# Kernel tuning notes

Measured on AMD Instinct MI355X. Metric: run time of the kernel, lower is better.

The kernel has to match this reference:

```python
import jax, jax.numpy as jnp
import numpy as np

LAG = 5
MSG_HID = 256
N_ATOMS = 30
N_EDGES = N_ATOMS * (N_ATOMS - 1)  # 870
BATCH = 2
T = 200


def _rel_matrices():
    # fully-connected directed graph, no self loops (standard NRI encoding)
    recv, send = [], []
    for i in range(N_ATOMS):
        for j in range(N_ATOMS):
            if i != j:
                recv.append(i)
                send.append(j)
    rel_rec = np.zeros((N_EDGES, N_ATOMS), dtype=np.float32)
    rel_send = np.zeros((N_EDGES, N_ATOMS), dtype=np.float32)
    rel_rec[np.arange(N_EDGES), recv] = 1.0
    rel_send[np.arange(N_EDGES), send] = 1.0
    return jnp.asarray(rel_rec), jnp.asarray(rel_send)


def setup_inputs() -> dict:
    key = jax.random.key(0)
    ks = jax.random.split(key, 14)
    rel_rec, rel_send = _rel_matrices()
    s = 0.05
    return {
        "inputs": jax.random.normal(ks[0], (BATCH, N_ATOMS, T), jnp.float32),
        "mu": jax.random.normal(ks[1], (BATCH, N_EDGES), jnp.float32),
        "logvar": jax.random.normal(ks[2], (BATCH, N_EDGES), jnp.float32) * 0.1,
        "eps": jax.random.normal(ks[3], (BATCH, N_EDGES), jnp.float32),
        "rel_rec": rel_rec,
        "rel_send": rel_send,
        "w_msg1": jax.random.normal(ks[4], (2 * LAG, MSG_HID), jnp.float32) * s,
        "b_msg1": jnp.zeros((MSG_HID,), jnp.float32),
        "w_msg2": jax.random.normal(ks[5], (MSG_HID, MSG_HID), jnp.float32) * s,
        "b_msg2": jnp.zeros((MSG_HID,), jnp.float32),
        "w_out1": jax.random.normal(ks[6], (LAG + MSG_HID, MSG_HID), jnp.float32) * s,
        "b_out1": jnp.zeros((MSG_HID,), jnp.float32),
        "w_out2": jax.random.normal(ks[7], (MSG_HID, MSG_HID), jnp.float32) * s,
        "b_out2": jnp.zeros((MSG_HID,), jnp.float32),
        "w_out3": jax.random.normal(ks[8], (MSG_HID, 1), jnp.float32) * s,
        "b_out3": jnp.zeros((1,), jnp.float32),
    }


def reference(inputs, mu, logvar, eps, rel_rec, rel_send,
              w_msg1, b_msg1, w_msg2, b_msg2,
              w_out1, b_out1, w_out2, b_out2, w_out3, b_out3):
    # reparametrize: edges [B, E]
    edges = eps * jnp.exp(0.5 * logvar) + mu

    # lag-stack: data [B, T-lag, N, lag]
    Tm = inputs.shape[2] - LAG
    data = jnp.stack([inputs[:, :, i:i + Tm] for i in range(LAG)], axis=-1)
    data = jnp.transpose(data, (0, 2, 1, 3))  # [B, Tm, N, lag]

    # gather node features to edges via one-hot matmuls
    receivers = jnp.einsum('en,btnl->btel', rel_rec, data)   # [B, Tm, E, lag]
    senders = jnp.einsum('en,btnl->btel', rel_send, data)    # [B, Tm, E, lag]
    pre_msg = jnp.concatenate([senders, receivers], axis=-1)  # [B, Tm, E, 2*lag]

    msg = jax.nn.relu(pre_msg @ w_msg1 + b_msg1)
    msg = jax.nn.relu(msg @ w_msg2 + b_msg2)                 # [B, Tm, E, hid]
    msg = msg * edges[:, None, :, None]                       # edge mask

    # scatter-aggregate messages back to receiver nodes
    agg_msgs = jnp.einsum('bteh,en->btnh', msg, rel_rec)      # [B, Tm, N, hid]

    aug = jnp.concatenate([data, agg_msgs], axis=-1)          # [B, Tm, N, lag+hid]
    pred = jax.nn.relu(aug @ w_out1 + b_out1)
    pred = jax.nn.relu(pred @ w_out2 + b_out2)
    pred = (pred @ w_out3 + b_out3)[..., 0]                   # [B, Tm, N]

    return jnp.transpose(pred, (0, 2, 1))                     # [B, N, Tm]
```

## Files before the change

### kernel.cpp

```cpp
#include <hip/hip_runtime.h>

#define LAG 5
#define HID 256
#define NA 30
#define NE 870
#define TM 195
#define TT 200
#define NB 2
#define EPN 29
#define TB3 65
#define NROWS (NB * TM * NA)
#define APAD 4
#define KC 32
#define UVB 1463
#define W2F_ELEMS (HID * HID)
#define W1F_ELEMS (HID * 288)
#define NWG2 (NB * NA * TB3)
#define Q8 (NWG2 / 8)
#define R8 (NWG2 % 8)

typedef _Float16 f16;
typedef _Float16 f16x8 __attribute__((ext_vector_type(8)));
typedef float floatx4 __attribute__((ext_vector_type(4)));
typedef float floatx16 __attribute__((ext_vector_type(16)));

__global__ __launch_bounds__(256) void k1_prep(
    const float* __restrict__ inputs, const float* __restrict__ w_msg1,
    const float* __restrict__ b_msg1, const float* __restrict__ w_msg2,
    const float* __restrict__ w_out1, const float* __restrict__ w_out2,
    f16* __restrict__ u, f16* __restrict__ v, f16* __restrict__ w2frag,
    f16* __restrict__ w1frag, f16* __restrict__ w2ofrag)
{
    const int bid = blockIdx.x, tid = threadIdx.x;
    if (bid < UVB) {
        __shared__ float feats8[8][LAG];
        const int r0 = bid * 8;
        if (tid < 8 * LAG) {
            const int i = tid / LAG, l = tid % LAG;
            const int r = r0 + i;
            float fv = 0.f;
            if (r < NROWS) {
                const int b = r / (TM * NA), rem = r % (TM * NA);
                const int t = rem / NA, n = rem % NA;
                fv = inputs[(b * NA + n) * TT + t + l];
            }
            feats8[i][l] = fv;
        }
        float w1c[2 * LAG];
        #pragma unroll
        for (int k = 0; k < 2 * LAG; ++k) w1c[k] = w_msg1[k * HID + tid];
        const float bb = b_msg1[tid];
        __syncthreads();
        const int c = tid >> 3, e = tid & 7;
        #pragma unroll
        for (int i = 0; i < 8; ++i) {
            const int r = r0 + i;
            if (r < NROWS) {
                float ua = bb, va = 0.f;
                #pragma unroll
                for (int l = 0; l < LAG; ++l) {
                    ua = fmaf(feats8[i][l], w1c[l], ua);
                    va = fmaf(feats8[i][l], w1c[LAG + l], va);
                }
                const int b = r / (TM * NA), rem = r % (TM * NA);
                const int t = rem / NA, n = rem % NA;
                const int base = ((b * TM + t) * 32 + c) * 240 + n * 8 + e;
                u[base] = (f16)ua;
                v[base] = (f16)va;
            }
        }
    } else if (bid < UVB + 32) {
        const int fidx = (bid - UVB) * 256 + tid;
        const int lane = fidx & 63;
        const int kc = (fidx >> 6) & 15;
        const int c32 = fidx >> 10;
        const int col = c32 * 32 + (lane & 31);
        const int kb = kc * 16 + (lane >> 5) * 8;
        f16x8 vv;
        #pragma unroll
        for (int x = 0; x < 8; ++x) vv[x] = (f16)w_msg2[(kb + x) * HID + col];
        *(f16x8*)&w2frag[fidx * 8] = vv;
    } else if (bid < UVB + 32 + 36) {
        const int fidx = (bid - (UVB + 32)) * 256 + tid;
        const int lane = fidx & 63;
        const int kc = (fidx >> 6) % 9;
        const int ntc = fidx / (64 * 9);
        const int col = ntc * 16 + (lane & 15);
        const int kb = kc * KC + (lane >> 4) * 8;
        f16x8 vv;
        #pragma unroll
        for (int x = 0; x < 8; ++x) {
            const int k = kb + x;
            float val;
            if (k < 256)      val = w_out1[(5 + k) * HID + col];
            else if (k < 261) val = w_out1[(k - 256) * HID + col];
            else              val = 0.f;
            vv[x] = (f16)val;
        }
        *(f16x8*)&w1frag[fidx * 8] = vv;
    } else {
        const int fidx = (bid - (UVB + 32 + 36)) * 256 + tid;
        const int lane = fidx & 63;
        const int kc = (fidx >> 6) & 7;
        const int ntc = fidx >> 9;
        const int col = ntc * 16 + (lane & 15);
        const int kb = kc * KC + (lane >> 4) * 8;
        f16x8 vv;
        #pragma unroll
        for (int x = 0; x < 8; ++x) vv[x] = (f16)w_out2[(kb + x) * HID + col];
        *(f16x8*)&w2ofrag[fidx * 8] = vv;
    }
}

__global__ __launch_bounds__(512, 4) void k2_msg(
    const f16* __restrict__ u, const f16* __restrict__ v,
    const f16* __restrict__ w2frag,
    const float* __restrict__ mu, const float* __restrict__ logvar,
    const float* __restrict__ eps, const float* __restrict__ b_msg2,
    f16* __restrict__ agg)
{
    __shared__ f16 a_lds[48 * 64 * 8];
    __shared__ float ev_lds[32];

    const int bid0 = blockIdx.x;
    const int xcd = bid0 & 7, sub = bid0 >> 3;
    const int bid = (xcd < R8 ? xcd * (Q8 + 1) : R8 * (Q8 + 1) + (xcd - R8) * Q8) + sub;

    const int n  = bid % NA;
    const int tb = (bid / NA) % TB3;
    const int b  = bid / (NA * TB3);
    const int t0 = tb * 3;
    const int tid = threadIdx.x;
    const int lane = tid & 63, w = tid >> 6;
    const int h = lane >> 5, l31 = lane & 31;

    if (tid < 32) {
        float evv = 0.f;
        if (tid < EPN) {
            const int e = b * NE + n * EPN + tid;
            evv = eps[e] * __expf(0.5f * logvar[e]) + mu[e];
        }
        ev_lds[tid] = evv;
    }

    const f16x8 z8 = {(f16)0, (f16)0, (f16)0, (f16)0, (f16)0, (f16)0, (f16)0, (f16)0};

    #pragma unroll
    for (int i = 0; i < 6; ++i) {
        const int task = i * 512 + tid;
        const int frag = task >> 6, fl = task & 63;
        const int tt = frag >> 4, kc = frag & 15;
        const int hh = fl >> 5, ei = fl & 31;
        const int c = kc * 2 + hh;
        const int rowbase = ((b * TM + t0 + tt) * 32 + c) * 240;
        f16x8 out8 = z8;
        if (ei < EPN) {
            const int j = ei + (ei >= n);
            const f16x8 uu = *(const f16x8*)(u + rowbase + j * 8);
            const f16x8 vv = *(const f16x8*)(v + rowbase + n * 8);
            out8 = __builtin_elementwise_max(uu + vv, z8);
        }
        *(f16x8*)&a_lds[task * 8] = out8;
    }

    const f16* bbase = w2frag + ((w * 16) << 9) + (lane << 3);
    f16x8 b0 = *(const f16x8*)(bbase + (0 << 9));
    f16x8 b1 = *(const f16x8*)(bbase + (1 << 9));
    f16x8 b2 = *(const f16x8*)(bbase + (2 << 9));

    floatx16 acc[3];
    #pragma unroll
    for (int mt = 0; mt < 3; ++mt)
        #pragma unroll
        for (int x = 0; x < 16; ++x) acc[mt][x] = 0.f;

    __syncthreads();

    #pragma unroll
    for (int kc = 0; kc < 16; ++kc) {
        f16x8 b3 = b2;
        if (kc < 13) b3 = *(const f16x8*)(bbase + ((kc + 3) << 9));
        f16x8 af[3];
        #pragma unroll
        for (int mt = 0; mt < 3; ++mt)
            af[mt] = *(const f16x8*)&a_lds[((mt * 16 + kc) * 64 + lane) * 8];
        __builtin_amdgcn_s_setprio(1);
        #pragma unroll
        for (int mt = 0; mt < 3; ++mt)
            acc[mt] = __builtin_amdgcn_mfma_f32_32x32x16_f16(af[mt], b0, acc[mt], 0, 0, 0);
        __builtin_amdgcn_s_setprio(0);
        b0 = b1; b1 = b2; b2 = b3;
    }

    float evr[16];
    #pragma unroll
    for (int reg = 0; reg < 16; ++reg)
        evr[reg] = ev_lds[(reg & 3) + 8 * (reg >> 2) + 4 * h];
    const float b2s = b_msg2[w * 32 + l31];

    #pragma unroll
    for (int mt = 0; mt < 3; ++mt) {
        const int t = t0 + mt;
        float part = 0.f;
        #pragma unroll
        for (int reg = 0; reg < 16; ++reg)
            part += evr[reg] * fmaxf(acc[mt][reg] + b2s, 0.f);
        part += __shfl_xor(part, 32, 64);
        if (h == 0)
            agg[(((b * TM + t) * NA + n) << 8) + w * 32 + l31] = (f16)part;
    }
}

__global__ __launch_bounds__(256) void k3_out(
    const f16* __restrict__ agg, const float* __restrict__ inputs,
    const f16* __restrict__ w1frag, const f16* __restrict__ w2ofrag,
    const float* __restrict__ b_out1, const float* __restrict__ b_out2,
    const float* __restrict__ w_out3, const float* __restrict__ b_out3,
    float* __restrict__ out)
{
    __shared__ f16 a1[16][288 + APAD];
    __shared__ float red[4][16];

    const int R0 = blockIdx.x * 16;
    const int tid = threadIdx.x;
    const int lane = tid & 63, w = tid >> 6;
    const int q = lane >> 4, m15 = lane & 15;
    const int wbase = w * 64;

    #pragma unroll
    for (int i = 0; i < 2; ++i) {
        const int task = i * 256 + tid;
        const int row = task >> 5, c = task & 31;
        const int R = R0 + row;
        f16x8 val;
        if (R < NROWS) {
            val = *(const f16x8*)&agg[(R << 8) + c * 8];
        } else {
            for (int x = 0; x < 8; ++x) val[x] = (f16)0.f;
        }
        *(f16x8*)&a1[row][c * 8] = val;
    }
    if (tid < 16) {
        const int R = R0 + tid;
        if (R < NROWS) {
            const int b = R / (TM * NA), rem = R % (TM * NA);
            const int t = rem / NA, n = rem % NA;
            const float* ip = inputs + (b * NA + n) * TT + t;
            #pragma unroll
            for (int l = 0; l < LAG; ++l) a1[tid][256 + l] = (f16)ip[l];
            #pragma unroll
            for (int k = 261; k < 288; ++k) a1[tid][k] = (f16)0.f;
        } else {
            for (int k = 256; k < 288; ++k) a1[tid][k] = (f16)0.f;
        }
    }

    floatx4 acc[4];
    #pragma unroll
    for (int nt = 0; nt < 4; ++nt) acc[nt] = (floatx4){0.f, 0.f, 0.f, 0.f};

    const f16* b1base = w1frag + (lane << 3);
    f16x8 bcur[4], bnxt[4];
    #pragma unroll
    for (int nt = 0; nt < 4; ++nt)
        bcur[nt] = *(const f16x8*)(b1base + (((w * 4 + nt) * 9 + 0) << 9));

    __syncthreads();

    #pragma unroll
    for (int kc = 0; kc < 9; ++kc) {
        if (kc < 8) {
            #pragma unroll
            for (int nt = 0; nt < 4; ++nt)
                bnxt[nt] = *(const f16x8*)(b1base + (((w * 4 + nt) * 9 + kc + 1) << 9));
        }
        const f16x8 af = *(const f16x8*)&a1[m15][kc * KC + q * 8];
        #pragma unroll
        for (int nt = 0; nt < 4; ++nt)
            acc[nt] = __builtin_amdgcn_mfma_f32_16x16x32_f16(af, bcur[nt], acc[nt], 0, 0, 0);
        #pragma unroll
        for (int nt = 0; nt < 4; ++nt) bcur[nt] = bnxt[nt];
    }
    __syncthreads();

    {
        float b1v[4];
        #pragma unroll
        for (int nt = 0; nt < 4; ++nt) b1v[nt] = b_out1[wbase + nt * 16 + m15];
        #pragma unroll
        for (int nt = 0; nt < 4; ++nt)
            #pragma unroll
            for (int reg = 0; reg < 4; ++reg)
                a1[q * 4 + reg][wbase + nt * 16 + m15] =
                    (f16)fmaxf(acc[nt][reg] + b1v[nt], 0.f);
    }

    #pragma unroll
    for (int nt = 0; nt < 4; ++nt) acc[nt] = (floatx4){0.f, 0.f, 0.f, 0.f};

    const f16* b2base = w2ofrag + (lane << 3);
    #pragma unroll
    for (int nt = 0; nt < 4; ++nt)
        bcur[nt] = *(const f16x8*)(b2base + (((w * 4 + nt) * 8 + 0) << 9));

    __syncthreads();

    #pragma unroll
    for (int kc = 0; kc < 8; ++kc) {
        if (kc < 7) {
            #pragma unroll
            for (int nt = 0; nt < 4; ++nt)
                bnxt[nt] = *(const f16x8*)(b2base + (((w * 4 + nt) * 8 + kc + 1) << 9));
        }
        const f16x8 af = *(const f16x8*)&a1[m15][kc * KC + q * 8];
        #pragma unroll
        for (int nt = 0; nt < 4; ++nt)
            acc[nt] = __builtin_amdgcn_mfma_f32_16x16x32_f16(af, bcur[nt], acc[nt], 0, 0, 0);
        #pragma unroll
        for (int nt = 0; nt < 4; ++nt) bcur[nt] = bnxt[nt];
    }

    {
        float b2v[4], w3v[4];
        #pragma unroll
        for (int nt = 0; nt < 4; ++nt) {
            const int col = wbase + nt * 16 + m15;
            b2v[nt] = b_out2[col];
            w3v[nt] = w_out3[col];
        }
        #pragma unroll
        for (int reg = 0; reg < 4; ++reg) {
            float p = 0.f;
            #pragma unroll
            for (int nt = 0; nt < 4; ++nt)
                p += fmaxf(acc[nt][reg] + b2v[nt], 0.f) * w3v[nt];
            p += __shfl_xor(p, 1, 64);
            p += __shfl_xor(p, 2, 64);
            p += __shfl_xor(p, 4, 64);
            p += __shfl_xor(p, 8, 64);
            if (m15 == 0) red[w][q * 4 + reg] = p;
        }
    }
    __syncthreads();
    if (tid < 16) {
        const int R = R0 + tid;
        if (R < NROWS) {
            const float val = red[0][tid] + red[1][tid] + red[2][tid] + red[3][tid] + b_out3[0];
            const int b = R / (TM * NA), rem = R % (TM * NA);
            const int t = rem / NA, n = rem % NA;
            out[(b * NA + n) * TM + t] = val;
        }
    }
}

extern "C" void kernel_launch(void* const* d_in, const int* in_sizes, int n_in,
                              void* d_out, int out_size, void* d_ws, size_t ws_size,
                              hipStream_t stream) {
    const float* inputs  = (const float*)d_in[0];
    const float* mu      = (const float*)d_in[1];
    const float* logvar  = (const float*)d_in[2];
    const float* eps     = (const float*)d_in[3];
    const float* w_msg1  = (const float*)d_in[6];
    const float* b_msg1  = (const float*)d_in[7];
    const float* w_msg2  = (const float*)d_in[8];
    const float* b_msg2  = (const float*)d_in[9];
    const float* w_out1  = (const float*)d_in[10];
    const float* b_out1  = (const float*)d_in[11];
    const float* w_out2  = (const float*)d_in[12];
    const float* b_out2  = (const float*)d_in[13];
    const float* w_out3  = (const float*)d_in[14];
    const float* b_out3  = (const float*)d_in[15];
    float* out = (float*)d_out;

    f16* u       = (f16*)d_ws;
    f16* v       = u       + NROWS * HID;
    f16* aggw    = v       + NROWS * HID;
    f16* w2frag  = aggw    + NROWS * HID;
    f16* w1frag  = w2frag  + W2F_ELEMS;
    f16* w2ofrag = w1frag  + W1F_ELEMS;

    hipLaunchKernelGGL(k1_prep, dim3(UVB + 32 + 36 + 32), dim3(256), 0, stream,
                       inputs, w_msg1, b_msg1, w_msg2, w_out1, w_out2,
                       u, v, w2frag, w1frag, w2ofrag);
    hipLaunchKernelGGL(k2_msg, dim3(NWG2), dim3(512), 0, stream,
                       u, v, w2frag, mu, logvar, eps, b_msg2, aggw);
    hipLaunchKernelGGL(k3_out, dim3((NROWS + 15) / 16), dim3(256), 0, stream,
                       aggw, inputs, w1frag, w2ofrag, b_out1, b_out2, w_out3, b_out3, out);
}
```

Baseline: 163.1 us.

## Retile message kernel to 2 timesteps per block with 2x2 MFMA tiles per wave

Restructures the message-MLP kernel so each block handles two timesteps with 256 threads instead of three timesteps with 512. Each wave now computes two 32-column output tiles for both timesteps, so every B fragment fetched from global memory feeds two MFMAs rather than one wave per column tile. The grid grows to 98 time blocks with a bounds guard for the padded last timestep, and the XCD remap drops its remainder handling. This trades more blocks and some wasted padded work for better B-fragment reuse and a different occupancy profile.

```diff
diff --git a/kernel.cpp b/kernel.cpp
--- a/kernel.cpp
+++ b/kernel.cpp
@@ -8,16 +8,15 @@
 #define TT 200
 #define NB 2
 #define EPN 29
-#define TB3 65
+#define TB2 98
 #define NROWS (NB * TM * NA)
 #define APAD 4
 #define KC 32
 #define UVB 1463
 #define W2F_ELEMS (HID * HID)
 #define W1F_ELEMS (HID * 288)
-#define NWG2 (NB * NA * TB3)
+#define NWG2 (NB * NA * TB2)
 #define Q8 (NWG2 / 8)
-#define R8 (NWG2 % 8)
 
 typedef _Float16 f16;
 typedef _Float16 f16x8 __attribute__((ext_vector_type(8)));
@@ -112,24 +111,23 @@
     }
 }
 
-__global__ __launch_bounds__(512, 4) void k2_msg(
+__global__ __launch_bounds__(256, 3) void k2_msg(
     const f16* __restrict__ u, const f16* __restrict__ v,
     const f16* __restrict__ w2frag,
     const float* __restrict__ mu, const float* __restrict__ logvar,
     const float* __restrict__ eps, const float* __restrict__ b_msg2,
     f16* __restrict__ agg)
 {
-    __shared__ f16 a_lds[48 * 64 * 8];
+    __shared__ f16 a_lds[32 * 64 * 8];
     __shared__ float ev_lds[32];
 
     const int bid0 = blockIdx.x;
-    const int xcd = bid0 & 7, sub = bid0 >> 3;
-    const int bid = (xcd < R8 ? xcd * (Q8 + 1) : R8 * (Q8 + 1) + (xcd - R8) * Q8) + sub;
+    const int bid = (bid0 & 7) * Q8 + (bid0 >> 3);
 
     const int n  = bid % NA;
-    const int tb = (bid / NA) % TB3;
-    const int b  = bid / (NA * TB3);
-    const int t0 = tb * 3;
+    const int tb = (bid / NA) % TB2;
+    const int b  = bid / (NA * TB2);
+    const int t0 = tb * 2;
     const int tid = threadIdx.x;
     const int lane = tid & 63, w = tid >> 6;
     const int h = lane >> 5, l31 = lane & 31;
@@ -146,15 +144,16 @@
     const f16x8 z8 = {(f16)0, (f16)0, (f16)0, (f16)0, (f16)0, (f16)0, (f16)0, (f16)0};
 
     #pragma unroll
-    for (int i = 0; i < 6; ++i) {
-        const int task = i * 512 + tid;
+    for (int i = 0; i < 8; ++i) {
+        const int task = i * 256 + tid;
         const int frag = task >> 6, fl = task & 63;
         const int tt = frag >> 4, kc = frag & 15;
         const int hh = fl >> 5, ei = fl & 31;
         const int c = kc * 2 + hh;
-        const int rowbase = ((b * TM + t0 + tt) * 32 + c) * 240;
+        const int t = t0 + tt;
         f16x8 out8 = z8;
-        if (ei < EPN) {
+        if (ei < EPN && t < TM) {
+            const int rowbase = ((b * TM + t) * 32 + c) * 240;
             const int j = ei + (ei >= n);
             const f16x8 uu = *(const f16x8*)(u + rowbase + j * 8);
             const f16x8 vv = *(const f16x8*)(v + rowbase + n * 8);
@@ -163,51 +162,70 @@
         *(f16x8*)&a_lds[task * 8] = out8;
     }
 
-    const f16* bbase = w2frag + ((w * 16) << 9) + (lane << 3);
-    f16x8 b0 = *(const f16x8*)(bbase + (0 << 9));
-    f16x8 b1 = *(const f16x8*)(bbase + (1 << 9));
-    f16x8 b2 = *(const f16x8*)(bbase + (2 << 9));
-
-    floatx16 acc[3];
-    #pragma unroll
-    for (int mt = 0; mt < 3; ++mt)
-        #pragma unroll
-        for (int x = 0; x < 16; ++x) acc[mt][x] = 0.f;
+    const f16* bb[2];
+    bb[0] = w2frag + (((2 * w + 0) * 16) << 9) + (lane << 3);
+    bb[1] = w2frag + (((2 * w + 1) * 16) << 9) + (lane << 3);
+    f16x8 b0[2], b1[2];
+    #pragma unroll
+    for (int nt = 0; nt < 2; ++nt) {
+        b0[nt] = *(const f16x8*)(bb[nt] + (0 << 9));
+        b1[nt] = *(const f16x8*)(bb[nt] + (1 << 9));
+    }
+
+    floatx16 acc[2][2];
+    #pragma unroll
+    for (int tt = 0; tt < 2; ++tt)
+        #pragma unroll
+        for (int nt = 0; nt < 2; ++nt)
+            #pragma unroll
+            for (int x = 0; x < 16; ++x) acc[tt][nt][x] = 0.f;
 
     __syncthreads();
 
     #pragma unroll
     for (int kc = 0; kc < 16; ++kc) {
-        f16x8 b3 = b2;
-        if (kc < 13) b3 = *(const f16x8*)(bbase + ((kc + 3) << 9));
-        f16x8 af[3];
-        #pragma unroll
-        for (int mt = 0; mt < 3; ++mt)
-            af[mt] = *(const f16x8*)&a_lds[((mt * 16 + kc) * 64 + lane) * 8];
+        f16x8 b2[2];
+        #pragma unroll
+        for (int nt = 0; nt < 2; ++nt) {
+            b2[nt] = b1[nt];
+            if (kc < 14) b2[nt] = *(const f16x8*)(bb[nt] + ((kc + 2) << 9));
+        }
+        f16x8 af[2];
+        #pragma unroll
+        for (int tt = 0; tt < 2; ++tt)
+            af[tt] = *(const f16x8*)&a_lds[((tt * 16 + kc) * 64 + lane) * 8];
         __builtin_amdgcn_s_setprio(1);
         #pragma unroll
-        for (int mt = 0; mt < 3; ++mt)
-            acc[mt] = __builtin_amdgcn_mfma_f32_32x32x16_f16(af[mt], b0, acc[mt], 0, 0, 0);
+        for (int nt = 0; nt < 2; ++nt)
+            #pragma unroll
+            for (int tt = 0; tt < 2; ++tt)
+                acc[tt][nt] = __builtin_amdgcn_mfma_f32_32x32x16_f16(af[tt], b0[nt], acc[tt][nt], 0, 0, 0);
         __builtin_amdgcn_s_setprio(0);
-        b0 = b1; b1 = b2; b2 = b3;
+        #pragma unroll
+        for (int nt = 0; nt < 2; ++nt) { b0[nt] = b1[nt]; b1[nt] = b2[nt]; }
     }
 
     float evr[16];
     #pragma unroll
     for (int reg = 0; reg < 16; ++reg)
         evr[reg] = ev_lds[(reg & 3) + 8 * (reg >> 2) + 4 * h];
-    const float b2s = b_msg2[w * 32 + l31];
-
-    #pragma unroll
-    for (int mt = 0; mt < 3; ++mt) {
-        const int t = t0 + mt;
-        float part = 0.f;
-        #pragma unroll
-        for (int reg = 0; reg < 16; ++reg)
-            part += evr[reg] * fmaxf(acc[mt][reg] + b2s, 0.f);
-        part += __shfl_xor(part, 32, 64);
-        if (h == 0)
-            agg[(((b * TM + t) * NA + n) << 8) + w * 32 + l31] = (f16)part;
+    float b2s[2];
+    #pragma unroll
+    for (int nt = 0; nt < 2; ++nt) b2s[nt] = b_msg2[(2 * w + nt) * 32 + l31];
+
+    #pragma unroll
+    for (int tt = 0; tt < 2; ++tt) {
+        const int t = t0 + tt;
+        #pragma unroll
+        for (int nt = 0; nt < 2; ++nt) {
+            float part = 0.f;
+            #pragma unroll
+            for (int reg = 0; reg < 16; ++reg)
+                part += evr[reg] * fmaxf(acc[tt][nt][reg] + b2s[nt], 0.f);
+            part += __shfl_xor(part, 32, 64);
+            if (h == 0 && t < TM)
+                agg[(((b * TM + t) * NA + n) << 8) + (2 * w + nt) * 32 + l31] = (f16)part;
+        }
     }
 }
 
@@ -382,7 +400,7 @@
     hipLaunchKernelGGL(k1_prep, dim3(UVB + 32 + 36 + 32), dim3(256), 0, stream,
                        inputs, w_msg1, b_msg1, w_msg2, w_out1, w_out2,
                        u, v, w2frag, w1frag, w2ofrag);
-    hipLaunchKernelGGL(k2_msg, dim3(NWG2), dim3(512), 0, stream,
+    hipLaunchKernelGGL(k2_msg, dim3(NWG2), dim3(256), 0, stream,
                        u, v, w2frag, mu, logvar, eps, b_msg2, aggw);
     hipLaunchKernelGGL(k3_out, dim3((NROWS + 15) / 16), dim3(256), 0, stream,
                        aggw, inputs, w1frag, w2ofrag, b_out1, b_out2, w_out3, b_out3, out);
```

Result: no change. 164.2 us (+0.7%).
